# Optimization experiments

Measured on AMD Instinct MI355X. Metric: run time of the kernel, lower is better.

The kernel has to match this reference:

```python
import math
import jax, jax.numpy as jnp
import numpy as np

B, A, U, S, E, HYP, H = 16384, 32, 64, 2048, 32, 64, 4
ATTEND_REG_COEF = 1e-3


def setup_inputs() -> dict:
    key = jax.random.key(0)
    ks = jax.random.split(key, 12)
    sc = 0.05
    return {
        "agent_qs": jax.random.normal(ks[0], (B, A), jnp.float32),
        "states": jax.random.normal(ks[1], (B, S), jnp.float32),
        # per-head selector hypernet: Linear(S,HYP)+ReLU+Linear(HYP,E,no bias)
        "sel_w1": jax.random.normal(ks[2], (H, S, HYP), jnp.float32) * sc,
        "sel_b1": jax.random.normal(ks[3], (H, HYP), jnp.float32) * sc,
        "sel_w2": jax.random.normal(ks[4], (H, HYP, E), jnp.float32) * sc,
        # per-head key extractor: Linear(U,E,no bias)
        "key_w": jax.random.normal(ks[5], (H, U, E), jnp.float32) * sc,
        # V net: Linear(S,E)+ReLU+Linear(E,1)
        "v_w1": jax.random.normal(ks[6], (S, E), jnp.float32) * sc,
        "v_b1": jax.random.normal(ks[7], (E,), jnp.float32) * sc,
        "v_w2": jax.random.normal(ks[8], (E, 1), jnp.float32) * sc,
        "v_b2": jax.random.normal(ks[9], (1,), jnp.float32) * sc,
    }


def reference(agent_qs, states, sel_w1, sel_b1, sel_w2, key_w, v_w1, v_b1, v_w2, v_b2):
    # nonlinear=False, weighted_head=False, state_bias=True (defaults used here)
    unit_states = states[:, : A * U].reshape(-1, A, U)  # [B, A, U]

    # per-head selectors: [B, H, E]
    h1 = jax.nn.relu(jnp.einsum("bs,hsk->bhk", states, sel_w1) + sel_b1[None])
    selectors = jnp.einsum("bhk,hke->bhe", h1, sel_w2)

    # per-head, per-agent keys: [B, H, A, E]
    keys = jnp.einsum("bau,hue->bhae", unit_states, key_w)

    # attention logits [B, H, A] (matches selector @ stacked-keys in torch)
    logits = jnp.einsum("bhe,bhae->bha", selectors, keys)
    weights = jax.nn.softmax(logits / math.sqrt(E), axis=-1)  # [B, H, A]

    head_attend = jnp.sum(weights, axis=1)  # [B, A]

    v = jax.nn.relu(states @ v_w1 + v_b1) @ v_w2 + v_b2  # [B, 1]

    # coef * sum over heads of mean(logits_h ** 2)
    attend_mag_regs = ATTEND_REG_COEF * jnp.sum(jnp.mean(logits ** 2, axis=(0, 2)))

    # per-head entropy: -(p * log(p + 1e-8)).sum(agents).mean(batch) -> [H]
    head_entropies = -jnp.mean(
        jnp.sum(weights * jnp.log(weights + 1e-8), axis=-1), axis=0
    )

    return head_attend, v, attend_mag_regs, head_entropies
```

## Files before the change

kernel.cpp:

```cpp
#include <hip/hip_runtime.h>
#include <hip/hip_bf16.h>

#define B_N 16384
#define A_N 32
#define U_N 64
#define S_N 2048
#define E_N 32
#define HYP_N 64
#define H_N 4
#define NREAL 288

#define WS_WT    0
#define WS_C1    1179648
#define WS_KWT   (WS_C1 + 9437184)
#define WS_PMAG  (WS_KWT + 32768)
#define WS_PENT  (WS_PMAG + 65536)

#define OUT_V   (B_N * A_N)
#define OUT_MAG (OUT_V + B_N)
#define OUT_ENT (OUT_MAG + 1)

typedef __attribute__((ext_vector_type(8))) short bf16x8_t;
typedef __attribute__((ext_vector_type(4))) float floatx4_t;

#define AS1(p) ((const __attribute__((address_space(1))) void*)(p))
#define AS3(p) ((__attribute__((address_space(3))) void*)(p))

__device__ __forceinline__ unsigned short f2b(float f) {
    union { float f; unsigned u; } v; v.f = f;
    unsigned r = v.u + 0x7FFFu + ((v.u >> 16) & 1u);
    return (unsigned short)(r >> 16);
}
__device__ __forceinline__ float b2f(unsigned x) {
    union { unsigned u; float f; } v; v.u = x << 16; return v.f;
}

__global__ __launch_bounds__(256) void pack_w_kernel(
        const float* __restrict__ sel_w1, const float* __restrict__ v_w1,
        const float* __restrict__ key_w,
        unsigned short* __restrict__ Wt, float* __restrict__ kwT) {
    int idx = blockIdx.x * 256 + threadIdx.x;
    if (idx < NREAL * S_N) {
        int n = idx >> 11;
        int k = idx & 2047;
        float val;
        if (n < 256) {
            int h = n >> 6, kk = n & 63;
            val = sel_w1[((size_t)h * S_N + k) * HYP_N + kk];
        } else {
            val = v_w1[(size_t)k * E_N + (n - 256)];
        }
        Wt[idx] = f2b(val);
    } else if (idx < NREAL * S_N + H_N * E_N * U_N) {
        int j = idx - NREAL * S_N;
        int h = j >> 11, e = (j >> 6) & 31, u = j & 63;
        kwT[j] = key_w[((size_t)h * U_N + u) * E_N + e];
    }
}

#define GM_BM 64
#define GM_BK 64

__global__ __launch_bounds__(256) void gemm2_kernel(
        const float* __restrict__ states, const unsigned short* __restrict__ Wt,
        const float* __restrict__ sel_b1, const float* __restrict__ v_b1,
        unsigned short* __restrict__ C1) {
    __shared__ __align__(16) unsigned short Asm[GM_BM * GM_BK];
    __shared__ __align__(16) unsigned short Bsm[NREAL * GM_BK];

    const int t = threadIdx.x;
    const int lane = t & 63;
    const int w = t >> 6;
    const int m0 = blockIdx.x * GM_BM;
    const int mw = (w >> 1) * 32;
    const int nw = (w & 1) * 144;

    floatx4_t acc[2][9] = {};

    for (int k0 = 0; k0 < S_N; k0 += GM_BK) {
        __syncthreads();

        float4 av[2][2];
#pragma unroll
        for (int i = 0; i < 2; ++i) {
            int p = i * 256 + t, r = p >> 3, cl = p & 7;
            const float* g = states + (size_t)(m0 + r) * S_N + k0 + cl * 8;
            av[i][0] = *(const float4*)g;
            av[i][1] = *(const float4*)(g + 4);
        }
#pragma unroll
        for (int i = 0; i < 9; ++i) {
            int p = i * 256 + t, n = p >> 3, sl = p & 7;
            int cl = sl ^ (n & 7);
            const unsigned short* g = Wt + (size_t)n * S_N + k0 + cl * 8;
            __builtin_amdgcn_global_load_lds(AS1(g), AS3(Bsm + p * 8), 16, 0, 0);
        }
#pragma unroll
        for (int i = 0; i < 2; ++i) {
            int p = i * 256 + t, r = p >> 3, cl = p & 7;
            int ph = cl ^ (r & 7);
            uint4 o;
            o.x = (unsigned)f2b(av[i][0].x) | ((unsigned)f2b(av[i][0].y) << 16);
            o.y = (unsigned)f2b(av[i][0].z) | ((unsigned)f2b(av[i][0].w) << 16);
            o.z = (unsigned)f2b(av[i][1].x) | ((unsigned)f2b(av[i][1].y) << 16);
            o.w = (unsigned)f2b(av[i][1].z) | ((unsigned)f2b(av[i][1].w) << 16);
            *(uint4*)(Asm + (size_t)(r * 8 + ph) * 8) = o;
        }
        __syncthreads();

#pragma unroll
        for (int s = 0; s < 2; ++s) {
            const int c = s * 4 + (lane >> 4);
            bf16x8_t afr[2];
#pragma unroll
            for (int mt = 0; mt < 2; ++mt) {
                int r = mw + mt * 16 + (lane & 15);
                int ph = c ^ (r & 7);
                afr[mt] = *(const bf16x8_t*)(Asm + r * 64 + ph * 8);
            }
#pragma unroll
            for (int nt = 0; nt < 9; ++nt) {
                int n = nw + nt * 16 + (lane & 15);
                int ph = c ^ (n & 7);
                bf16x8_t bfr = *(const bf16x8_t*)(Bsm + n * 64 + ph * 8);
                acc[0][nt] = __builtin_amdgcn_mfma_f32_16x16x32_bf16(
                    afr[0], bfr, acc[0][nt], 0, 0, 0);
                acc[1][nt] = __builtin_amdgcn_mfma_f32_16x16x32_bf16(
                    afr[1], bfr, acc[1][nt], 0, 0, 0);
            }
        }
    }

#pragma unroll
    for (int nt = 0; nt < 9; ++nt) {
        int n = nw + nt * 16 + (lane & 15);
        float bias = (n < 256) ? sel_b1[n] : v_b1[n - 256];
#pragma unroll
        for (int mt = 0; mt < 2; ++mt) {
            int rbase = m0 + mw + mt * 16 + (lane >> 4) * 4;
#pragma unroll
            for (int rg = 0; rg < 4; ++rg) {
                float v = acc[mt][nt][rg] + bias;
                C1[(size_t)(rbase + rg) * NREAL + n] = f2b(v > 0.0f ? v : 0.0f);
            }
        }
    }
}

__global__ __launch_bounds__(256) void epilogue2_kernel(
        const float* __restrict__ states, const unsigned short* __restrict__ C1,
        const float* __restrict__ sel_w2, const float* __restrict__ kwT,
        const float* __restrict__ v_w2, const float* __restrict__ v_b2,
        float* __restrict__ out, float* __restrict__ pmag, float* __restrict__ pent) {
    __shared__ float us[4][A_N * 65];
    __shared__ float h1s[4][NREAL];
    __shared__ float sel_s[4][H_N * E_N];
    __shared__ float ts[4][H_N * U_N];

    const int t = threadIdx.x;
    const int w = t >> 6;
    const int lane = t & 63;
    const int b = blockIdx.x * 4 + w;

    {
        const float4* src = (const float4*)(states + (size_t)b * S_N);
#pragma unroll
        for (int i = 0; i < 8; ++i) {
            int f = i * 64 + lane;
            float4 v4 = src[f];
            int a = f >> 4, u = (f & 15) << 2;
            float* d = &us[w][a * 65 + u];
            d[0] = v4.x; d[1] = v4.y; d[2] = v4.z; d[3] = v4.w;
        }
    }
    if (lane < 36) {
        uint4 v = *(const uint4*)(C1 + (size_t)b * NREAL + lane * 8);
        float* d = &h1s[w][lane * 8];
        d[0] = b2f(v.x & 0xffff); d[1] = b2f(v.x >> 16);
        d[2] = b2f(v.y & 0xffff); d[3] = b2f(v.y >> 16);
        d[4] = b2f(v.z & 0xffff); d[5] = b2f(v.z >> 16);
        d[6] = b2f(v.w & 0xffff); d[7] = b2f(v.w >> 16);
    }
    __syncthreads();

#pragma unroll
    for (int l = 0; l < 2; ++l) {
        int idx = l * 64 + lane, h = idx >> 5, e = idx & 31;
        const float* hh = &h1s[w][h * HYP_N];
        const float* w2 = sel_w2 + (size_t)h * HYP_N * E_N + e;
        float s = 0.0f;
#pragma unroll
        for (int k = 0; k < HYP_N; ++k) s = fmaf(hh[k], w2[(size_t)k * E_N], s);
        sel_s[w][idx] = s;
    }
    __syncthreads();

#pragma unroll
    for (int l = 0; l < 4; ++l) {
        int idx = l * 64 + lane, h = idx >> 6, u = idx & 63;
        const float* sh = &sel_s[w][h * E_N];
        const float* kw = kwT + (size_t)h * E_N * U_N + u;
        float s = 0.0f;
#pragma unroll
        for (int e = 0; e < E_N; ++e) s = fmaf(sh[e], kw[(size_t)e * U_N], s);
        ts[w][idx] = s;
    }
    __syncthreads();

    float wgt[2];
    float mag = 0.0f;
#pragma unroll
    for (int l = 0; l < 2; ++l) {
        int idx = l * 64 + lane, h = idx >> 5, a = idx & 31;
        const float* ua = &us[w][a * 65];
        const float* th = &ts[w][h * U_N];
        float lg = 0.0f;
#pragma unroll
        for (int u = 0; u < U_N; ++u) lg = fmaf(ua[u], th[u], lg);
        mag += lg * lg;

        float x = lg * 0.17677669529663687f;
        float m = x;
#pragma unroll
        for (int o = 16; o > 0; o >>= 1) m = fmaxf(m, __shfl_xor(m, o, 32));
        float p = expf(x - m);
        float den = p;
#pragma unroll
        for (int o = 16; o > 0; o >>= 1) den += __shfl_xor(den, o, 32);
        float wv = p / den;
        wgt[l] = wv;

        float ent = wv * logf(wv + 1e-8f);
#pragma unroll
        for (int o = 16; o > 0; o >>= 1) ent += __shfl_xor(ent, o, 32);
        if (a == 0) pent[(size_t)h * B_N + b] = ent;
    }

#pragma unroll
    for (int o = 32; o > 0; o >>= 1) mag += __shfl_xor(mag, o, 64);
    if (lane == 0) pmag[b] = mag;

    float partial = wgt[0] + wgt[1];
    partial += __shfl_xor(partial, 32, 64);
    if (lane < 32) out[(size_t)b * A_N + lane] = partial;

    if (lane < 32) {
        float p = h1s[w][256 + lane] * v_w2[lane];
#pragma unroll
        for (int o = 16; o > 0; o >>= 1) p += __shfl_xor(p, o, 32);
        if (lane == 0) out[OUT_V + b] = p + v_b2[0];
    }
}

__global__ __launch_bounds__(256) void finalize_kernel(
        const float* __restrict__ pmag, const float* __restrict__ pent,
        float* __restrict__ out) {
    int which = blockIdx.x;
    const float* src = (which == 0) ? pmag : (pent + (size_t)(which - 1) * B_N);
    float s = 0.0f;
    for (int i = threadIdx.x; i < B_N; i += 256) s += src[i];
#pragma unroll
    for (int o = 32; o > 0; o >>= 1) s += __shfl_xor(s, o, 64);
    __shared__ float red[4];
    if ((threadIdx.x & 63) == 0) red[threadIdx.x >> 6] = s;
    __syncthreads();
    if (threadIdx.x == 0) {
        float tot = red[0] + red[1] + red[2] + red[3];
        if (which == 0) out[OUT_MAG] = 1e-3f * tot / (float)(B_N * A_N);
        else out[OUT_ENT + which - 1] = -tot / (float)B_N;
    }
}

extern "C" void kernel_launch(void* const* d_in, const int* in_sizes, int n_in,
                              void* d_out, int out_size, void* d_ws, size_t ws_size,
                              hipStream_t stream) {
    const float* states = (const float*)d_in[1];
    const float* sel_w1 = (const float*)d_in[2];
    const float* sel_b1 = (const float*)d_in[3];
    const float* sel_w2 = (const float*)d_in[4];
    const float* key_w  = (const float*)d_in[5];
    const float* v_w1   = (const float*)d_in[6];
    const float* v_b1   = (const float*)d_in[7];
    const float* v_w2   = (const float*)d_in[8];
    const float* v_b2   = (const float*)d_in[9];
    float* out = (float*)d_out;
    char* wsb  = (char*)d_ws;

    unsigned short* Wt  = (unsigned short*)(wsb + WS_WT);
    unsigned short* C1  = (unsigned short*)(wsb + WS_C1);
    float* kwT          = (float*)(wsb + WS_KWT);
    float* pmag         = (float*)(wsb + WS_PMAG);
    float* pent         = (float*)(wsb + WS_PENT);

    pack_w_kernel<<<dim3((NREAL * S_N + H_N * E_N * U_N + 255) / 256), dim3(256), 0, stream>>>(
        sel_w1, v_w1, key_w, Wt, kwT);
    gemm2_kernel<<<dim3(B_N / GM_BM), dim3(256), 0, stream>>>(
        states, Wt, sel_b1, v_b1, C1);
    epilogue2_kernel<<<dim3(B_N / 4), dim3(256), 0, stream>>>(
        states, C1, sel_w2, kwT, v_w2, v_b2, out, pmag, pent);
    finalize_kernel<<<dim3(5), dim3(256), 0, stream>>>(pmag, pent, out);
}
```

Measured before the change: 318.9 us.

## Fold sel_w2·key_w into one matrix, use MFMA epilogue and prefetching GEMM

```diff
diff --git a/kernel.cpp b/kernel.cpp
--- a/kernel.cpp
+++ b/kernel.cpp
@@ -9,11 +9,12 @@
 #define HYP_N 64
 #define H_N 4
 #define NREAL 288
+#define NPADG 320
 
 #define WS_WT    0
-#define WS_C1    1179648
-#define WS_KWT   (WS_C1 + 9437184)
-#define WS_PMAG  (WS_KWT + 32768)
+#define WS_C1    1310720
+#define WS_MB    (WS_C1 + 9437184)
+#define WS_PMAG  (WS_MB + 32768)
 #define WS_PENT  (WS_PMAG + 65536)
 
 #define OUT_V   (B_N * A_N)
@@ -37,77 +38,80 @@
 
 __global__ __launch_bounds__(256) void pack_w_kernel(
         const float* __restrict__ sel_w1, const float* __restrict__ v_w1,
-        const float* __restrict__ key_w,
-        unsigned short* __restrict__ Wt, float* __restrict__ kwT) {
+        const float* __restrict__ sel_w2, const float* __restrict__ key_w,
+        unsigned short* __restrict__ Wt, unsigned short* __restrict__ Mb) {
     int idx = blockIdx.x * 256 + threadIdx.x;
-    if (idx < NREAL * S_N) {
+    if (idx < NPADG * S_N) {
         int n = idx >> 11;
         int k = idx & 2047;
-        float val;
+        float val = 0.0f;
         if (n < 256) {
             int h = n >> 6, kk = n & 63;
             val = sel_w1[((size_t)h * S_N + k) * HYP_N + kk];
-        } else {
+        } else if (n < NREAL) {
             val = v_w1[(size_t)k * E_N + (n - 256)];
         }
         Wt[idx] = f2b(val);
-    } else if (idx < NREAL * S_N + H_N * E_N * U_N) {
-        int j = idx - NREAL * S_N;
-        int h = j >> 11, e = (j >> 6) & 31, u = j & 63;
-        kwT[j] = key_w[((size_t)h * U_N + u) * E_N + e];
+    } else if (idx < NPADG * S_N + H_N * U_N * HYP_N) {
+        int j = idx - NPADG * S_N;
+        int h = j >> 12, u = (j >> 6) & 63, k = j & 63;
+        const float* kw = key_w + ((size_t)h * U_N + u) * E_N;
+        const float* w2 = sel_w2 + ((size_t)h * HYP_N + k) * E_N;
+        float s = 0.0f;
+#pragma unroll
+        for (int e = 0; e < E_N; ++e) s = fmaf(kw[e], w2[e], s);
+        Mb[j] = f2b(s);
     }
 }
 
 #define GM_BM 64
 #define GM_BK 64
 
-__global__ __launch_bounds__(256) void gemm2_kernel(
+__global__ __launch_bounds__(512) void gemm3_kernel(
         const float* __restrict__ states, const unsigned short* __restrict__ Wt,
         const float* __restrict__ sel_b1, const float* __restrict__ v_b1,
         unsigned short* __restrict__ C1) {
     __shared__ __align__(16) unsigned short Asm[GM_BM * GM_BK];
-    __shared__ __align__(16) unsigned short Bsm[NREAL * GM_BK];
+    __shared__ __align__(16) unsigned short Bsm[NPADG * GM_BK];
 
     const int t = threadIdx.x;
     const int lane = t & 63;
     const int w = t >> 6;
     const int m0 = blockIdx.x * GM_BM;
-    const int mw = (w >> 1) * 32;
-    const int nw = (w & 1) * 144;
-
-    floatx4_t acc[2][9] = {};
-
-    for (int k0 = 0; k0 < S_N; k0 += GM_BK) {
-        __syncthreads();
-
-        float4 av[2][2];
-#pragma unroll
-        for (int i = 0; i < 2; ++i) {
-            int p = i * 256 + t, r = p >> 3, cl = p & 7;
-            const float* g = states + (size_t)(m0 + r) * S_N + k0 + cl * 8;
-            av[i][0] = *(const float4*)g;
-            av[i][1] = *(const float4*)(g + 4);
-        }
-#pragma unroll
-        for (int i = 0; i < 9; ++i) {
-            int p = i * 256 + t, n = p >> 3, sl = p & 7;
-            int cl = sl ^ (n & 7);
-            const unsigned short* g = Wt + (size_t)n * S_N + k0 + cl * 8;
-            __builtin_amdgcn_global_load_lds(AS1(g), AS3(Bsm + p * 8), 16, 0, 0);
-        }
-#pragma unroll
-        for (int i = 0; i < 2; ++i) {
-            int p = i * 256 + t, r = p >> 3, cl = p & 7;
-            int ph = cl ^ (r & 7);
-            uint4 o;
-            o.x = (unsigned)f2b(av[i][0].x) | ((unsigned)f2b(av[i][0].y) << 16);
-            o.y = (unsigned)f2b(av[i][0].z) | ((unsigned)f2b(av[i][0].w) << 16);
-            o.z = (unsigned)f2b(av[i][1].x) | ((unsigned)f2b(av[i][1].y) << 16);
-            o.w = (unsigned)f2b(av[i][1].z) | ((unsigned)f2b(av[i][1].w) << 16);
-            *(uint4*)(Asm + (size_t)(r * 8 + ph) * 8) = o;
-        }
-        __syncthreads();
-
+    const int mw = (w & 1) * 32;
+    const int nw = (w >> 1) * 80;
+
+    const int ar = t >> 3, acl = t & 7;
+    const float* ap = states + (size_t)(m0 + ar) * S_N + acl * 8;
+
+    floatx4_t acc[2][5] = {};
+
+    float4 a0 = *(const float4*)(ap);
+    float4 a1 = *(const float4*)(ap + 4);
+    {
+        int ph = acl ^ (ar & 7);
+        uint4 o;
+        o.x = (unsigned)f2b(a0.x) | ((unsigned)f2b(a0.y) << 16);
+        o.y = (unsigned)f2b(a0.z) | ((unsigned)f2b(a0.w) << 16);
+        o.z = (unsigned)f2b(a1.x) | ((unsigned)f2b(a1.y) << 16);
+        o.w = (unsigned)f2b(a1.z) | ((unsigned)f2b(a1.w) << 16);
+        *(uint4*)(Asm + (size_t)(ar * 8 + ph) * 8) = o;
+    }
+#pragma unroll
+    for (int i = 0; i < 5; ++i) {
+        int p = i * 512 + t, n = p >> 3, sl = p & 7;
+        int cl = sl ^ (n & 7);
+        __builtin_amdgcn_global_load_lds(AS1(Wt + (size_t)n * S_N + cl * 8),
+                                         AS3(Bsm + p * 8), 16, 0, 0);
+    }
+    __syncthreads();
+
+    for (int it = 0; it < 32; ++it) {
+        if (it < 31) {
+            const float* g = ap + (it + 1) * GM_BK;
+            a0 = *(const float4*)(g);
+            a1 = *(const float4*)(g + 4);
+        }
 #pragma unroll
         for (int s = 0; s < 2; ++s) {
             const int c = s * 4 + (lane >> 4);
@@ -119,7 +123,7 @@
                 afr[mt] = *(const bf16x8_t*)(Asm + r * 64 + ph * 8);
             }
 #pragma unroll
-            for (int nt = 0; nt < 9; ++nt) {
+            for (int nt = 0; nt < 5; ++nt) {
                 int n = nw + nt * 16 + (lane & 15);
                 int ph = c ^ (n & 7);
                 bf16x8_t bfr = *(const bf16x8_t*)(Bsm + n * 64 + ph * 8);
@@ -129,11 +133,34 @@
                     afr[1], bfr, acc[1][nt], 0, 0, 0);
             }
         }
-    }
-
-#pragma unroll
-    for (int nt = 0; nt < 9; ++nt) {
+        __syncthreads();
+        if (it < 31) {
+            int k0 = (it + 1) * GM_BK;
+            {
+                int ph = acl ^ (ar & 7);
+                uint4 o;
+                o.x = (unsigned)f2b(a0.x) | ((unsigned)f2b(a0.y) << 16);
+                o.y = (unsigned)f2b(a0.z) | ((unsigned)f2b(a0.w) << 16);
+                o.z = (unsigned)f2b(a1.x) | ((unsigned)f2b(a1.y) << 16);
+                o.w = (unsigned)f2b(a1.z) | ((unsigned)f2b(a1.w) << 16);
+                *(uint4*)(Asm + (size_t)(ar * 8 + ph) * 8) = o;
+            }
+#pragma unroll
+            for (int i = 0; i < 5; ++i) {
+                int p = i * 512 + t, n = p >> 3, sl = p & 7;
+                int cl = sl ^ (n & 7);
+                __builtin_amdgcn_global_load_lds(
+                    AS1(Wt + (size_t)n * S_N + k0 + cl * 8),
+                    AS3(Bsm + p * 8), 16, 0, 0);
+            }
+            __syncthreads();
+        }
+    }
+
+#pragma unroll
+    for (int nt = 0; nt < 5; ++nt) {
         int n = nw + nt * 16 + (lane & 15);
+        if (n >= NREAL) continue;
         float bias = (n < 256) ? sel_b1[n] : v_b1[n - 256];
 #pragma unroll
         for (int mt = 0; mt < 2; ++mt) {
@@ -147,108 +174,138 @@
     }
 }
 
-__global__ __launch_bounds__(256) void epilogue2_kernel(
+#define EP_ROWS 32
+#define H1_STRIDE 312
+#define TS_STRIDE 260
+
+__global__ __launch_bounds__(256) void epilogue3_kernel(
         const float* __restrict__ states, const unsigned short* __restrict__ C1,
-        const float* __restrict__ sel_w2, const float* __restrict__ kwT,
+        const unsigned short* __restrict__ Mb,
         const float* __restrict__ v_w2, const float* __restrict__ v_b2,
         float* __restrict__ out, float* __restrict__ pmag, float* __restrict__ pent) {
-    __shared__ float us[4][A_N * 65];
-    __shared__ float h1s[4][NREAL];
-    __shared__ float sel_s[4][H_N * E_N];
-    __shared__ float ts[4][H_N * U_N];
+    __shared__ __align__(16) unsigned short h1s[EP_ROWS][H1_STRIDE];
+    __shared__ float ts[EP_ROWS][TS_STRIDE];
 
     const int t = threadIdx.x;
     const int w = t >> 6;
     const int lane = t & 63;
-    const int b = blockIdx.x * 4 + w;
+    const int b0 = blockIdx.x * EP_ROWS;
+
+#pragma unroll
+    for (int i = 0; i < 5; ++i) {
+        int c = i * 256 + t;
+        if (c < EP_ROWS * 36) {
+            int r = c / 36, cc = c - r * 36;
+            int n = cc * 8;
+            uint4 v = *(const uint4*)(C1 + (size_t)(b0 + r) * NREAL + n);
+            int idx = (n < 256) ? ((n >> 6) * 72 + (n & 63))
+                                : (((n - 256) >> 3) * 72 + 64);
+            *(uint4*)&h1s[r][idx] = v;
+        }
+    }
+    __syncthreads();
 
     {
-        const float4* src = (const float4*)(states + (size_t)b * S_N);
-#pragma unroll
-        for (int i = 0; i < 8; ++i) {
-            int f = i * 64 + lane;
-            float4 v4 = src[f];
-            int a = f >> 4, u = (f & 15) << 2;
-            float* d = &us[w][a * 65 + u];
-            d[0] = v4.x; d[1] = v4.y; d[2] = v4.z; d[3] = v4.w;
-        }
-    }
-    if (lane < 36) {
-        uint4 v = *(const uint4*)(C1 + (size_t)b * NREAL + lane * 8);
-        float* d = &h1s[w][lane * 8];
-        d[0] = b2f(v.x & 0xffff); d[1] = b2f(v.x >> 16);
-        d[2] = b2f(v.y & 0xffff); d[3] = b2f(v.y >> 16);
-        d[4] = b2f(v.z & 0xffff); d[5] = b2f(v.z >> 16);
-        d[6] = b2f(v.w & 0xffff); d[7] = b2f(v.w >> 16);
+        const int h = w;
+        floatx4_t tacc[2][4] = {};
+#pragma unroll
+        for (int s = 0; s < 2; ++s) {
+            int k0 = s * 32 + (lane >> 4) * 8;
+            bf16x8_t bfr[4];
+#pragma unroll
+            for (int ut = 0; ut < 4; ++ut) {
+                int u = ut * 16 + (lane & 15);
+                bfr[ut] = *(const bf16x8_t*)(Mb + ((size_t)(h * U_N + u) * 64) + k0);
+            }
+#pragma unroll
+            for (int mt = 0; mt < 2; ++mt) {
+                int r = mt * 16 + (lane & 15);
+                bf16x8_t afr = *(const bf16x8_t*)&h1s[r][h * 72 + k0];
+#pragma unroll
+                for (int ut = 0; ut < 4; ++ut)
+                    tacc[mt][ut] = __builtin_amdgcn_mfma_f32_16x16x32_bf16(
+                        afr, bfr[ut], tacc[mt][ut], 0, 0, 0);
+            }
+        }
+#pragma unroll
+        for (int mt = 0; mt < 2; ++mt)
+#pragma unroll
+            for (int ut = 0; ut < 4; ++ut)
+#pragma unroll
+                for (int rg = 0; rg < 4; ++rg) {
+                    int r = mt * 16 + (lane >> 4) * 4 + rg;
+                    int u = ut * 16 + (lane & 15);
+                    ts[r][h * U_N + u] = tacc[mt][ut][rg];
+                }
     }
     __syncthreads();
 
-#pragma unroll
-    for (int l = 0; l < 2; ++l) {
-        int idx = l * 64 + lane, h = idx >> 5, e = idx & 31;
-        const float* hh = &h1s[w][h * HYP_N];
-        const float* w2 = sel_w2 + (size_t)h * HYP_N * E_N + e;
-        float s = 0.0f;
-#pragma unroll
-        for (int k = 0; k < HYP_N; ++k) s = fmaf(hh[k], w2[(size_t)k * E_N], s);
-        sel_s[w][idx] = s;
-    }
-    __syncthreads();
-
-#pragma unroll
-    for (int l = 0; l < 4; ++l) {
-        int idx = l * 64 + lane, h = idx >> 6, u = idx & 63;
-        const float* sh = &sel_s[w][h * E_N];
-        const float* kw = kwT + (size_t)h * E_N * U_N + u;
-        float s = 0.0f;
-#pragma unroll
-        for (int e = 0; e < E_N; ++e) s = fmaf(sh[e], kw[(size_t)e * U_N], s);
-        ts[w][idx] = s;
-    }
-    __syncthreads();
-
-    float wgt[2];
-    float mag = 0.0f;
-#pragma unroll
-    for (int l = 0; l < 2; ++l) {
-        int idx = l * 64 + lane, h = idx >> 5, a = idx & 31;
-        const float* ua = &us[w][a * 65];
-        const float* th = &ts[w][h * U_N];
-        float lg = 0.0f;
-#pragma unroll
-        for (int u = 0; u < U_N; ++u) lg = fmaf(ua[u], th[u], lg);
-        mag += lg * lg;
-
-        float x = lg * 0.17677669529663687f;
-        float m = x;
-#pragma unroll
-        for (int o = 16; o > 0; o >>= 1) m = fmaxf(m, __shfl_xor(m, o, 32));
-        float p = expf(x - m);
-        float den = p;
-#pragma unroll
-        for (int o = 16; o > 0; o >>= 1) den += __shfl_xor(den, o, 32);
-        float wv = p / den;
-        wgt[l] = wv;
-
-        float ent = wv * logf(wv + 1e-8f);
-#pragma unroll
-        for (int o = 16; o > 0; o >>= 1) ent += __shfl_xor(ent, o, 32);
-        if (a == 0) pent[(size_t)h * B_N + b] = ent;
-    }
-
-#pragma unroll
-    for (int o = 32; o > 0; o >>= 1) mag += __shfl_xor(mag, o, 64);
-    if (lane == 0) pmag[b] = mag;
-
-    float partial = wgt[0] + wgt[1];
-    partial += __shfl_xor(partial, 32, 64);
-    if (lane < 32) out[(size_t)b * A_N + lane] = partial;
-
-    if (lane < 32) {
-        float p = h1s[w][256 + lane] * v_w2[lane];
-#pragma unroll
-        for (int o = 16; o > 0; o >>= 1) p += __shfl_xor(p, o, 32);
-        if (lane == 0) out[OUT_V + b] = p + v_b2[0];
+    const int a = lane & 31, uh = lane >> 5;
+    float4 cur[8], nxt[8];
+    {
+        const float* up = states + (size_t)(b0 + w * 8) * S_N + a * 64 + uh * 32;
+#pragma unroll
+        for (int i = 0; i < 8; ++i) cur[i] = ((const float4*)up)[i];
+    }
+    for (int rr = 0; rr < 8; ++rr) {
+        int r = w * 8 + rr;
+        int b = b0 + r;
+        if (rr < 7) {
+            const float* up = states + (size_t)(b + 1) * S_N + a * 64 + uh * 32;
+#pragma unroll
+            for (int i = 0; i < 8; ++i) nxt[i] = ((const float4*)up)[i];
+        }
+        float pl[4];
+#pragma unroll
+        for (int h = 0; h < 4; ++h) {
+            const float* tp = &ts[r][h * U_N + uh * 32];
+            float s = 0.0f;
+#pragma unroll
+            for (int i = 0; i < 8; ++i) {
+                float4 t4 = *(const float4*)(tp + i * 4);
+                s = fmaf(cur[i].x, t4.x, s);
+                s = fmaf(cur[i].y, t4.y, s);
+                s = fmaf(cur[i].z, t4.z, s);
+                s = fmaf(cur[i].w, t4.w, s);
+            }
+            pl[h] = s + __shfl_xor(s, 32, 64);
+        }
+        float mg = pl[0]*pl[0] + pl[1]*pl[1] + pl[2]*pl[2] + pl[3]*pl[3];
+#pragma unroll
+        for (int o = 16; o > 0; o >>= 1) mg += __shfl_xor(mg, o, 32);
+        float hatt = 0.0f;
+        float entv[4];
+#pragma unroll
+        for (int h = 0; h < 4; ++h) {
+            float x = pl[h] * 0.17677669529663687f;
+            float m = x;
+#pragma unroll
+            for (int o = 16; o > 0; o >>= 1) m = fmaxf(m, __shfl_xor(m, o, 32));
+            float p = expf(x - m);
+            float den = p;
+#pragma unroll
+            for (int o = 16; o > 0; o >>= 1) den += __shfl_xor(den, o, 32);
+            float wv = p / den;
+            hatt += wv;
+            float e = wv * logf(wv + 1e-8f);
+#pragma unroll
+            for (int o = 16; o > 0; o >>= 1) e += __shfl_xor(e, o, 32);
+            entv[h] = e;
+        }
+        if (uh == 0) {
+            out[(size_t)b * A_N + a] = hatt;
+            float pv = b2f((unsigned)h1s[r][(a >> 3) * 72 + 64 + (a & 7)]) * v_w2[a];
+#pragma unroll
+            for (int o = 16; o > 0; o >>= 1) pv += __shfl_xor(pv, o, 32);
+            if (a == 0) {
+                out[OUT_V + b] = pv + v_b2[0];
+                pmag[b] = mg;
+#pragma unroll
+                for (int h = 0; h < 4; ++h) pent[(size_t)h * B_N + b] = entv[h];
+            }
+        }
+#pragma unroll
+        for (int i = 0; i < 8; ++i) cur[i] = nxt[i];
     }
 }
 
@@ -288,15 +345,15 @@
 
     unsigned short* Wt  = (unsigned short*)(wsb + WS_WT);
     unsigned short* C1  = (unsigned short*)(wsb + WS_C1);
-    float* kwT          = (float*)(wsb + WS_KWT);
+    unsigned short* Mb  = (unsigned short*)(wsb + WS_MB);
     float* pmag         = (float*)(wsb + WS_PMAG);
     float* pent         = (float*)(wsb + WS_PENT);
 
-    pack_w_kernel<<<dim3((NREAL * S_N + H_N * E_N * U_N + 255) / 256), dim3(256), 0, stream>>>(
-        sel_w1, v_w1, key_w, Wt, kwT);
-    gemm2_kernel<<<dim3(B_N / GM_BM), dim3(256), 0, stream>>>(
+    pack_w_kernel<<<dim3((NPADG * S_N + H_N * U_N * HYP_N + 255) / 256),
+                    dim3(256), 0, stream>>>(sel_w1, v_w1, sel_w2, key_w, Wt, Mb);
+    gemm3_kernel<<<dim3(B_N / GM_BM), dim3(512), 0, stream>>>(
         states, Wt, sel_b1, v_b1, C1);
-    epilogue2_kernel<<<dim3(B_N / 4), dim3(256), 0, stream>>>(
-        states, C1, sel_w2, kwT, v_w2, v_b2, out, pmag, pent);
+    epilogue3_kernel<<<dim3(B_N / EP_ROWS), dim3(256), 0, stream>>>(
+        states, C1, Mb, v_w2, v_b2, out, pmag, pent);
     finalize_kernel<<<dim3(5), dim3(256), 0, stream>>>(pmag, pent, out);
 }
```

Result: faster. 295.7 us (-7.3%).
